# Performance work log

Measured on AMD Instinct MI355X. Metric: run time of the kernel, lower is better.

Reference implementation:

```python
import jax, jax.numpy as jnp
import numpy as np

N = 50000      # num_nodes
E = 800000     # num_edges (avg degree 16)
IC, OC = 2, 2  # in_channels, out_channels
DIN, DOUT = 128, 128
K = 3          # number of hops


def setup_inputs() -> dict:
    key = jax.random.key(0)
    k1, k2, k3, k4 = jax.random.split(key, 4)
    x = jax.random.normal(k1, (IC, N, DIN), dtype=jnp.float32)
    edge_index = jax.random.randint(k2, (2, E), 0, N, dtype=jnp.int32)
    a = np.sqrt(6.0 / (DIN + DOUT)).astype(np.float32)  # xavier_uniform bound
    W = jax.random.uniform(k3, (OC, IC, DIN, DOUT), minval=-a, maxval=a, dtype=jnp.float32)
    params = jax.random.uniform(k4, (OC, IC, K + 1), minval=0.0, maxval=0.01, dtype=jnp.float32)
    return {"x": x, "edge_index": edge_index, "W": W, "params": params}


def reference(x, edge_index, W, params):
    # x: [IC, N, DIN]; edge_index: [2, E]; W: [OC, IC, DIN, DOUT]; params: [OC, IC, K+1]
    n = x.shape[1]
    k_hops = params.shape[-1] - 1
    row, col = edge_index[0], edge_index[1]

    # normalize_adj: symmetric D^-1/2 A D^-1/2 on unit-valued edges
    deg = jax.ops.segment_sum(jnp.ones(row.shape[0], x.dtype), row, num_segments=n)
    dinv = jnp.where(deg > 0, jax.lax.rsqrt(deg), jnp.zeros_like(deg))
    val = dinv[row] * dinv[col]  # [E]

    def spmm(X):  # A_norm @ X per channel; X: [IC, N, d]
        gathered = X[:, col, :] * val[None, :, None]  # [IC, E, d]
        return jax.vmap(lambda g: jax.ops.segment_sum(g, row, num_segments=n))(gathered)

    # Hop features: H[m] = A^m x, computed once (hoisting the redundant spmm in the torch loop)
    hops = [x]
    for _ in range(k_hops):
        hops.append(spmm(hops[-1]))
    H = jnp.stack(hops)  # [K+1, IC, N, DIN]

    # out[i] = sum_j sum_m params[i,j,m] * (A^m x_j) @ W[i,j]
    return jnp.einsum('mjnd,ijm,ijdf->inf', H, params, W)  # [OC, N, DOUT]
```

## Files before the change

kernel.cpp:

```cpp
#include <hip/hip_runtime.h>
#include <hip/hip_bf16.h>
#include <stdint.h>

#define NN 50000
#define NE 800000
#define D 128
#define KH 3
#define SCAN_B ((NN + 255) / 256)

typedef __attribute__((ext_vector_type(8))) __bf16 bf16x8;
typedef __attribute__((ext_vector_type(4))) float f32x4;

__device__ __forceinline__ uint16_t bf16_rne(float f) {
  uint32_t u = __builtin_bit_cast(uint32_t, f);
  u = (u + 0x7fffu + ((u >> 16) & 1u)) >> 16;
  return (uint16_t)u;
}
__device__ __forceinline__ uint32_t bf16_pack(float lo, float hi) {
  return ((uint32_t)bf16_rne(hi) << 16) | (uint32_t)bf16_rne(lo);
}

#define GLDS16(gp, lp)                                                         \
  __builtin_amdgcn_global_load_lds(                                            \
      (__attribute__((address_space(1))) void*)(gp),                           \
      (__attribute__((address_space(3))) void*)(lp), 16, 0, 0)

__global__ void k_deg(const int* __restrict__ row, int* __restrict__ deg) {
  int e = blockIdx.x * 256 + threadIdx.x;
  if (e < NE) atomicAdd(&deg[row[e]], 1);
}

__global__ void k_dinv_bsum(const int* __restrict__ deg, float* __restrict__ dinv,
                            int* __restrict__ bsum) {
  __shared__ int s[256];
  int t = threadIdx.x;
  int i = blockIdx.x * 256 + t;
  int d = (i < NN) ? deg[i] : 0;
  if (i < NN) dinv[i] = (d > 0) ? rsqrtf((float)d) : 0.0f;
  s[t] = d;
  __syncthreads();
  for (int off = 128; off > 0; off >>= 1) {
    if (t < off) s[t] += s[t + off];
    __syncthreads();
  }
  if (t == 0) bsum[blockIdx.x] = s[0];
}

__global__ void k_rpwrite(const int* __restrict__ deg, const int* __restrict__ bsum,
                          int* __restrict__ rp, int* __restrict__ cur) {
  __shared__ int s[256];
  __shared__ int sboff;
  int t = threadIdx.x;
  int b = blockIdx.x;
  int pv = (t < b) ? bsum[t] : 0;
  s[t] = pv;
  __syncthreads();
  for (int off = 128; off > 0; off >>= 1) {
    if (t < off) s[t] += s[t + off];
    __syncthreads();
  }
  if (t == 0) sboff = s[0];
  __syncthreads();
  int i = b * 256 + t;
  int v = (i < NN) ? deg[i] : 0;
  s[t] = v;
  __syncthreads();
  for (int off = 1; off < 256; off <<= 1) {
    int u = (t >= off) ? s[t - off] : 0;
    __syncthreads();
    s[t] += u;
    __syncthreads();
  }
  if (i < NN) {
    int r = sboff + s[t] - v;
    rp[i] = r;
    cur[i] = r;
  }
  if (i == 0) rp[NN] = NE;
}

__global__ void k_scatter(const int* __restrict__ row, const int* __restrict__ col,
                          const float* __restrict__ dinv, int* __restrict__ cur,
                          int2* __restrict__ csr) {
  int e = blockIdx.x * 256 + threadIdx.x;
  if (e < NE) {
    int r = row[e], c = col[e];
    int pos = atomicAdd(&cur[r], 1);
    csr[pos] = make_int2(c, __float_as_int(dinv[r] * dinv[c]));
  }
}

#define XB 6250
__global__ void k_prep_c(const float* __restrict__ x, const float* __restrict__ W,
                         const float* __restrict__ params, uint16_t* __restrict__ dst,
                         uint16_t* __restrict__ wb) {
  int b = blockIdx.x, t = threadIdx.x;
  if (b < XB) {
    int base = (b * 256 + t) * 8;
    int n = base >> 8, c0 = base & 255;
    int j = c0 >> 7, dd = c0 & 127;
    const float* xp = x + (size_t)j * NN * D + (size_t)n * D + dd;
    float4 f0 = *(const float4*)xp;
    float4 f1 = *(const float4*)(xp + 4);
    uint4 o;
    o.x = bf16_pack(f0.x, f0.y);
    o.y = bf16_pack(f0.z, f0.w);
    o.z = bf16_pack(f1.x, f1.y);
    o.w = bf16_pack(f1.z, f1.w);
    *(uint4*)(dst + base) = o;
  } else {
    int idx = (b - XB) * 256 + t;
    int c = idx >> 10, k = idx & 1023;
    int i = c >> 7, f = c & 127, m = k >> 8, j = (k >> 7) & 1, dd = k & 127;
    float p = params[(i * 2 + j) * 4 + m];
    float w = W[((i * 2 + j) * 128 + dd) * 128 + f];
    wb[idx] = bf16_rne(p * w);
  }
}

__global__ void k_wbig_f(const float* __restrict__ W, const float* __restrict__ params,
                         uint16_t* __restrict__ wb) {
  int idx = blockIdx.x * 256 + threadIdx.x;
  if (idx >= 2 * 256 * 512) return;
  int j = idx >> 17, c = (idx >> 9) & 255, k = idx & 511;
  int i = c >> 7, f = c & 127, m = k >> 7, dd = k & 127;
  float p = params[(i * 2 + j) * 4 + m];
  float w = W[((i * 2 + j) * 128 + dd) * 128 + f];
  wb[idx] = bf16_rne(p * w);
}

__global__ void k_x2h_f(const float* __restrict__ xj, uint16_t* __restrict__ dst) {
  int idx = blockIdx.x * 256 + threadIdx.x;
  if (idx < NN * D) dst[idx] = bf16_rne(xj[idx]);
}

template <int NCH>
__global__ void k_spmm(const int* __restrict__ rp, const int2* __restrict__ csr,
                       const uint16_t* __restrict__ src, uint16_t* __restrict__ dst) {
  constexpr int STRIDE = NCH * 128;
  typedef uint32_t gvec __attribute__((ext_vector_type(NCH)));
  const int lane = threadIdx.x & 63;
  const int wid = threadIdx.x >> 6;
  const int r = blockIdx.x * 4 + wid;
  if (r >= NN) return;
  const int s = __builtin_amdgcn_readfirstlane(rp[r]);
  const int e = __builtin_amdgcn_readfirstlane(rp[r + 1]);
  const int lo = lane * 2 * NCH;

  float a[2 * NCH] = {};
  for (int i = s; i < e; i += 8) {
    int2 cv[8];
    gvec g[8];
#pragma unroll
    for (int u = 0; u < 8; ++u) {
      int idx = i + u;
      bool ok = idx < e;
      cv[u] = csr[ok ? idx : e - 1];
      if (!ok) cv[u].y = 0;
    }
#pragma unroll
    for (int u = 0; u < 8; ++u)
      g[u] = *(const gvec*)(src + (size_t)cv[u].x * STRIDE + lo);
#pragma unroll
    for (int u = 0; u < 8; ++u) {
      float v = __int_as_float(cv[u].y);
#pragma unroll
      for (int q = 0; q < NCH; ++q) {
        a[2 * q] = fmaf(v, __builtin_bit_cast(float, g[u][q] << 16), a[2 * q]);
        a[2 * q + 1] =
            fmaf(v, __builtin_bit_cast(float, g[u][q] & 0xffff0000u), a[2 * q + 1]);
      }
    }
  }
  gvec o;
#pragma unroll
  for (int q = 0; q < NCH; ++q) o[q] = bf16_pack(a[2 * q], a[2 * q + 1]);
  *(gvec*)(dst + (size_t)r * STRIDE + lo) = o;
}

template <int KTOT, int HOPW, int ACCUM>
__global__ __launch_bounds__(256) void k_gemm(
    const uint16_t* __restrict__ h0, const uint16_t* __restrict__ h1,
    const uint16_t* __restrict__ h2, const uint16_t* __restrict__ h3,
    const uint16_t* __restrict__ wb, float* __restrict__ out) {
  __shared__ __align__(16) uint16_t As[128 * 64];
  __shared__ __align__(16) uint16_t Bs[128 * 64];
  const uint16_t* hops[4] = {h0, h1, h2, h3};
  int t = threadIdx.x;
  int lane = t & 63, wid = t >> 6;
  int wm = wid >> 1, wn = wid & 1;
  int m0 = blockIdx.x * 128;
  int c0 = blockIdx.y * 128;
  int rl = lane & 15, q = lane >> 4;
  f32x4 acc[4][4] = {};
#pragma unroll
  for (int hop = 0; hop < KTOT / HOPW; ++hop) {
    const uint16_t* hm = hops[hop];
#pragma unroll
    for (int kin = 0; kin < HOPW; kin += 64) {
      int k0 = hop * HOPW + kin;
#pragma unroll
      for (int rr = 0; rr < 4; ++rr) {
        int c = rr * 256 + t;
        int row = c >> 3, kcL = c & 7;
        int kcG = kcL ^ (row & 7);
        int gr = m0 + row;
        gr = gr < NN ? gr : NN - 1;
        GLDS16(hm + (size_t)gr * HOPW + kin + kcG * 8, &As[c * 8]);
      }
#pragma unroll
      for (int rr = 0; rr < 4; ++rr) {
        int c = rr * 256 + t;
        int cc = c >> 3, kcL = c & 7;
        int kcG = kcL ^ (cc & 7);
        GLDS16(wb + (size_t)(c0 + cc) * KTOT + k0 + kcG * 8, &Bs[c * 8]);
      }
      __syncthreads();
#pragma unroll
      for (int kq2 = 0; kq2 < 2; ++kq2) {
        int w = kq2 * 4 + q;
        bf16x8 af[4], bq[4];
#pragma unroll
        for (int f = 0; f < 4; ++f) {
          int row = wm * 64 + f * 16 + rl;
          af[f] = *(const bf16x8*)(&As[row * 64 + (w ^ (row & 7)) * 8]);
          int col = wn * 64 + f * 16 + rl;
          bq[f] = *(const bf16x8*)(&Bs[col * 64 + (w ^ (col & 7)) * 8]);
        }
#pragma unroll
        for (int fm = 0; fm < 4; ++fm)
#pragma unroll
          for (int fn = 0; fn < 4; ++fn)
            acc[fm][fn] = __builtin_amdgcn_mfma_f32_16x16x32_bf16(af[fm], bq[fn],
                                                                  acc[fm][fn], 0, 0, 0);
      }
      __syncthreads();
    }
  }
  int iOut = blockIdx.y;
#pragma unroll
  for (int fm = 0; fm < 4; ++fm) {
#pragma unroll
    for (int r = 0; r < 4; ++r) {
      int rowg = m0 + wm * 64 + fm * 16 + q * 4 + r;
      if (rowg >= NN) continue;
      float* op = out + ((size_t)iOut * NN + rowg) * D;
#pragma unroll
      for (int fn = 0; fn < 4; ++fn) {
        int colg = wn * 64 + fn * 16 + rl;
        if (ACCUM)
          op[colg] += acc[fm][fn][r];
        else
          op[colg] = acc[fm][fn][r];
      }
    }
  }
}

extern "C" void kernel_launch(void* const* d_in, const int* in_sizes, int n_in,
                              void* d_out, int out_size, void* d_ws, size_t ws_size,
                              hipStream_t stream) {
  (void)in_sizes; (void)n_in; (void)out_size;
  const float* x = (const float*)d_in[0];
  const int* ei = (const int*)d_in[1];
  const float* W = (const float*)d_in[2];
  const float* params = (const float*)d_in[3];
  float* out = (float*)d_out;
  char* ws = (char*)d_ws;

  size_t off = 0;
  auto take = [&](size_t bytes) {
    char* p = ws + off;
    off = (off + bytes + 255) & ~(size_t)255;
    return p;
  };
  int* deg = (int*)take((size_t)NN * 4);
  float* dinv = (float*)take((size_t)NN * 4);
  int* rp = (int*)take((size_t)(NN + 1) * 4);
  int* cur = (int*)take((size_t)NN * 4);
  int* bsum = (int*)take(256 * 4);
  int2* csr = (int2*)take((size_t)NE * 8);
  uint16_t* wb = (uint16_t*)take((size_t)256 * 1024 * 2);
  size_t fixed = off;

  hipMemsetAsync(deg, 0, (size_t)NN * 4, stream);
  k_deg<<<(NE + 255) / 256, 256, 0, stream>>>(ei, deg);
  k_dinv_bsum<<<SCAN_B, 256, 0, stream>>>(deg, dinv, bsum);
  k_rpwrite<<<SCAN_B, 256, 0, stream>>>(deg, bsum, rp, cur);
  k_scatter<<<(NE + 255) / 256, 256, 0, stream>>>(ei, ei + NE, dinv, cur, csr);

  size_t hopC = (size_t)NN * 256 * 2;
  size_t needC = fixed + 4 * hopC + 1024;

  if (ws_size >= needC) {
    uint16_t* hop[4];
    for (int m = 0; m < 4; ++m) hop[m] = (uint16_t*)take(hopC);
    k_prep_c<<<XB + 1024, 256, 0, stream>>>(x, W, params, hop[0], wb);
    for (int m = 1; m <= KH; ++m)
      k_spmm<2><<<(NN + 3) / 4, 256, 0, stream>>>(rp, csr, hop[m - 1], hop[m]);
    dim3 grid((NN + 127) / 128, 2);
    k_gemm<1024, 256, 0><<<grid, 256, 0, stream>>>(hop[0], hop[1], hop[2], hop[3],
                                                   wb, out);
  } else {
    size_t hopF = (size_t)NN * 128 * 2;
    uint16_t* hop[4];
    for (int m = 0; m < 4; ++m) hop[m] = (uint16_t*)take(hopF);
    k_wbig_f<<<(2 * 256 * 512 + 255) / 256, 256, 0, stream>>>(W, params, wb);
    for (int j = 0; j < 2; ++j) {
      k_x2h_f<<<(NN * D + 255) / 256, 256, 0, stream>>>(x + (size_t)j * NN * D, hop[0]);
      for (int m = 1; m <= KH; ++m)
        k_spmm<1><<<(NN + 3) / 4, 256, 0, stream>>>(rp, csr, hop[m - 1], hop[m]);
      dim3 grid((NN + 127) / 128, 2);
      if (j == 0)
        k_gemm<512, 128, 0><<<grid, 256, 0, stream>>>(hop[0], hop[1], hop[2], hop[3],
                                                      wb, out);
      else
        k_gemm<512, 128, 1><<<grid, 256, 0, stream>>>(hop[0], hop[1], hop[2], hop[3],
                                                      wb + 256 * 512, out);
    }
  }
}
```

Before: 391.4 us.

## Split SpMM rows across eight column groups with edge-parallel lanes

Replaces the row-per-wave SpMM in the main path with a kernel that launches eight times as many blocks. Each block handles one 32-column slice of a row, and within a wave eight edges are processed in parallel, eight lanes per edge. Partial sums are then reduced with cross-lane shuffles. The aim is more parallelism and better latency hiding for the irregular gathers. The cost is that each CSR entry is reloaded once per column group, each gather is only 8 bytes wide, and a shuffle reduction is added per row.

```diff
diff --git a/kernel.cpp b/kernel.cpp
--- a/kernel.cpp
+++ b/kernel.cpp
@@ -178,6 +178,47 @@
   *(gvec*)(dst + (size_t)r * STRIDE + lo) = o;
 }
 
+__global__ void k_spmm_g(const int* __restrict__ rp, const long long* __restrict__ csr,
+                         const uint16_t* __restrict__ src, uint16_t* __restrict__ dst) {
+  const int lane = threadIdx.x & 63;
+  const int wid = threadIdx.x >> 6;
+  const int g = blockIdx.x & 7;
+  const int r = (blockIdx.x >> 3) * 4 + wid;
+  if (r >= NN) return;
+  const int s = __builtin_amdgcn_readfirstlane(rp[r]);
+  const int e = __builtin_amdgcn_readfirstlane(rp[r + 1]);
+  const int oct = lane >> 3;
+  const int cp = lane & 7;
+  const int co = g * 32 + cp * 4;
+
+  float a0 = 0.f, a1 = 0.f, a2 = 0.f, a3 = 0.f;
+  for (int i = s; i < e; i += 8) {
+    int idx = i + oct;
+    bool ok = idx < e;
+    long long cvp = __builtin_nontemporal_load(&csr[ok ? idx : e - 1]);
+    int cx = (int)(uint32_t)(cvp & 0xffffffffll);
+    float v = ok ? __int_as_float((int)(cvp >> 32)) : 0.0f;
+    uint2 gd = *(const uint2*)(src + (size_t)cx * 256 + co);
+    a0 = fmaf(v, __builtin_bit_cast(float, gd.x << 16), a0);
+    a1 = fmaf(v, __builtin_bit_cast(float, gd.x & 0xffff0000u), a1);
+    a2 = fmaf(v, __builtin_bit_cast(float, gd.y << 16), a2);
+    a3 = fmaf(v, __builtin_bit_cast(float, gd.y & 0xffff0000u), a3);
+  }
+#pragma unroll
+  for (int m = 8; m < 64; m <<= 1) {
+    a0 += __shfl_xor(a0, m);
+    a1 += __shfl_xor(a1, m);
+    a2 += __shfl_xor(a2, m);
+    a3 += __shfl_xor(a3, m);
+  }
+  if (lane < 8) {
+    uint2 o;
+    o.x = bf16_pack(a0, a1);
+    o.y = bf16_pack(a2, a3);
+    *(uint2*)(dst + (size_t)r * 256 + co) = o;
+  }
+}
+
 template <int KTOT, int HOPW, int ACCUM>
 __global__ __launch_bounds__(256) void k_gemm(
     const uint16_t* __restrict__ h0, const uint16_t* __restrict__ h1,
@@ -283,7 +324,7 @@
   uint16_t* wb = (uint16_t*)take((size_t)256 * 1024 * 2);
   size_t fixed = off;
 
-  hipMemsetAsync(deg, 0, (size_t)NN * 4, stream);
+  (void)hipMemsetAsync(deg, 0, (size_t)NN * 4, stream);
   k_deg<<<(NE + 255) / 256, 256, 0, stream>>>(ei, deg);
   k_dinv_bsum<<<SCAN_B, 256, 0, stream>>>(deg, dinv, bsum);
   k_rpwrite<<<SCAN_B, 256, 0, stream>>>(deg, bsum, rp, cur);
@@ -297,7 +338,8 @@
     for (int m = 0; m < 4; ++m) hop[m] = (uint16_t*)take(hopC);
     k_prep_c<<<XB + 1024, 256, 0, stream>>>(x, W, params, hop[0], wb);
     for (int m = 1; m <= KH; ++m)
-      k_spmm<2><<<(NN + 3) / 4, 256, 0, stream>>>(rp, csr, hop[m - 1], hop[m]);
+      k_spmm_g<<<8 * ((NN + 3) / 4), 256, 0, stream>>>(
+          rp, (const long long*)csr, hop[m - 1], hop[m]);
     dim3 grid((NN + 127) / 128, 2);
     k_gemm<1024, 256, 0><<<grid, 256, 0, stream>>>(hop[0], hop[1], hop[2], hop[3],
                                                    wb, out);
```

Result: slower. 803.3 us (+105.2%).

## Replace GEMM with 64-row tile kernel covering both outputs per block

Applied to the files above, without the earlier changes.

Adds a new GEMM kernel in which each block takes 64 node rows and computes all 256 output columns (both output channels) at once. The old kernel used a 2D grid of 128-row tiles, with a separate block per output channel. The new layout reads the A tile (hop features) from global memory once for both outputs, halving that traffic, and produces more, smaller blocks for better load balance. In exchange each block loads a larger B tile per k-step and has less reuse of W per row.

```diff
diff --git a/kernel.cpp b/kernel.cpp
--- a/kernel.cpp
+++ b/kernel.cpp
@@ -257,6 +257,83 @@
   }
 }
 
+__global__ __launch_bounds__(256) void k_gemm2(
+    const uint16_t* __restrict__ h0, const uint16_t* __restrict__ h1,
+    const uint16_t* __restrict__ h2, const uint16_t* __restrict__ h3,
+    const uint16_t* __restrict__ wb, float* __restrict__ out) {
+  __shared__ __align__(16) uint16_t As[64 * 64];
+  __shared__ __align__(16) uint16_t Bs[256 * 64];
+  const uint16_t* hops[4] = {h0, h1, h2, h3};
+  int t = threadIdx.x;
+  int lane = t & 63, wid = t >> 6;
+  int wn = wid;
+  int m0 = blockIdx.x * 64;
+  int rl = lane & 15, q = lane >> 4;
+  f32x4 acc[4][4] = {};
+#pragma unroll
+  for (int hop = 0; hop < 4; ++hop) {
+    const uint16_t* hm = hops[hop];
+#pragma unroll
+    for (int kin = 0; kin < 256; kin += 64) {
+      int k0 = hop * 256 + kin;
+      {
+#pragma unroll
+        for (int rr = 0; rr < 2; ++rr) {
+          int c = rr * 256 + t;
+          int row = c >> 3, kcL = c & 7;
+          int kcG = kcL ^ (row & 7);
+          int gr = m0 + row;
+          gr = gr < NN ? gr : NN - 1;
+          GLDS16(hm + (size_t)gr * 256 + kin + kcG * 8, &As[c * 8]);
+        }
+      }
+      {
+#pragma unroll
+        for (int rr = 0; rr < 8; ++rr) {
+          int c = rr * 256 + t;
+          int cc = c >> 3, kcL = c & 7;
+          int kcG = kcL ^ (cc & 7);
+          GLDS16(wb + (size_t)cc * 1024 + k0 + kcG * 8, &Bs[c * 8]);
+        }
+      }
+      __syncthreads();
+#pragma unroll
+      for (int kq2 = 0; kq2 < 2; ++kq2) {
+        int w = kq2 * 4 + q;
+        bf16x8 af[4], bq[4];
+#pragma unroll
+        for (int f = 0; f < 4; ++f) {
+          int row = f * 16 + rl;
+          af[f] = *(const bf16x8*)(&As[row * 64 + (w ^ (row & 7)) * 8]);
+          int col = wn * 64 + f * 16 + rl;
+          bq[f] = *(const bf16x8*)(&Bs[col * 64 + (w ^ (col & 7)) * 8]);
+        }
+#pragma unroll
+        for (int fm = 0; fm < 4; ++fm)
+#pragma unroll
+          for (int fn = 0; fn < 4; ++fn)
+            acc[fm][fn] = __builtin_amdgcn_mfma_f32_16x16x32_bf16(af[fm], bq[fn],
+                                                                  acc[fm][fn], 0, 0, 0);
+      }
+      __syncthreads();
+    }
+  }
+#pragma unroll
+  for (int fm = 0; fm < 4; ++fm) {
+#pragma unroll
+    for (int r = 0; r < 4; ++r) {
+      int rowg = m0 + fm * 16 + q * 4 + r;
+      if (rowg >= NN) continue;
+#pragma unroll
+      for (int fn = 0; fn < 4; ++fn) {
+        int col = wn * 64 + fn * 16 + rl;
+        int iOut = col >> 7, colg = col & 127;
+        out[((size_t)iOut * NN + rowg) * D + colg] = acc[fm][fn][r];
+      }
+    }
+  }
+}
+
 extern "C" void kernel_launch(void* const* d_in, const int* in_sizes, int n_in,
                               void* d_out, int out_size, void* d_ws, size_t ws_size,
                               hipStream_t stream) {
@@ -283,7 +360,7 @@
   uint16_t* wb = (uint16_t*)take((size_t)256 * 1024 * 2);
   size_t fixed = off;
 
-  hipMemsetAsync(deg, 0, (size_t)NN * 4, stream);
+  (void)hipMemsetAsync(deg, 0, (size_t)NN * 4, stream);
   k_deg<<<(NE + 255) / 256, 256, 0, stream>>>(ei, deg);
   k_dinv_bsum<<<SCAN_B, 256, 0, stream>>>(deg, dinv, bsum);
   k_rpwrite<<<SCAN_B, 256, 0, stream>>>(deg, bsum, rp, cur);
@@ -298,9 +375,8 @@
     k_prep_c<<<XB + 1024, 256, 0, stream>>>(x, W, params, hop[0], wb);
     for (int m = 1; m <= KH; ++m)
       k_spmm<2><<<(NN + 3) / 4, 256, 0, stream>>>(rp, csr, hop[m - 1], hop[m]);
-    dim3 grid((NN + 127) / 128, 2);
-    k_gemm<1024, 256, 0><<<grid, 256, 0, stream>>>(hop[0], hop[1], hop[2], hop[3],
-                                                   wb, out);
+    k_gemm2<<<(NN + 63) / 64, 256, 0, stream>>>(hop[0], hop[1], hop[2], hop[3],
+                                                wb, out);
   } else {
     size_t hopF = (size_t)NN * 128 * 2;
     uint16_t* hop[4];
```

Measured after the change: 391.8 us. Within noise of the previous version (+0.1%).
